# Performance work log

Measured on AMD Instinct MI355X. Metric: run time of the kernel, lower is better.

Reference implementation:

```python
import jax, jax.numpy as jnp
import numpy as np

HIDDEN = 1024
B, S = 4, 2048


def setup_inputs() -> dict:
    key = jax.random.key(0)
    ks = jax.random.split(key, 8)
    scale = 1.0 / np.sqrt(HIDDEN)
    return {
        "hidden_states": jax.random.normal(ks[0], (B, S, HIDDEN), dtype=jnp.float32),
        "attention_mask": jnp.zeros((B, S, S), dtype=jnp.float32),
        "Wq": jax.random.normal(ks[1], (HIDDEN, HIDDEN), dtype=jnp.float32) * scale,
        "bq": jnp.zeros((HIDDEN,), dtype=jnp.float32),
        "Wk": jax.random.normal(ks[2], (HIDDEN, HIDDEN), dtype=jnp.float32) * scale,
        "bk": jnp.zeros((HIDDEN,), dtype=jnp.float32),
        "Wv": jax.random.normal(ks[3], (HIDDEN, HIDDEN), dtype=jnp.float32) * scale,
        "bv": jnp.zeros((HIDDEN,), dtype=jnp.float32),
    }


def reference(hidden_states, attention_mask, Wq, bq, Wk, bk, Wv, bv):
    # Dense projections (note: no head split in the original module)
    q = jnp.einsum('bsd,de->bse', hidden_states, Wq) + bq  # [B,S,H]
    k = jnp.einsum('bsd,de->bse', hidden_states, Wk) + bk
    v = jnp.einsum('bsd,de->bse', hidden_states, Wv) + bv
    # scores scaled by sqrt(hidden_size) (not per-head dim), per the source
    inv_scale = 1.0 / jnp.sqrt(jnp.asarray(q.shape[-1], dtype=q.dtype))
    scores = jnp.einsum('bqd,bkd->bqk', q, k) * inv_scale  # [B,S,S]
    scores = scores + attention_mask
    weights = jax.nn.softmax(scores, axis=-1)
    # dropout is identity (training=False)
    out = jnp.einsum('bqk,bkd->bqd', weights, v)  # [B,S,H]
    return out
```

## Files before the change

kernel.cpp:

```cpp
#include <hip/hip_runtime.h>
#include <stdint.h>

typedef __attribute__((ext_vector_type(8))) short short8;
typedef __attribute__((ext_vector_type(8))) unsigned short u16x8;
typedef __attribute__((ext_vector_type(4))) float f32x4;

__device__ __forceinline__ uint16_t f2bf(float x) {
  uint32_t u = __float_as_uint(x);
  uint32_t r = (u + 0x7FFFu + ((u >> 16) & 1u)) >> 16;
  return (uint16_t)r;
}
__device__ __forceinline__ float bf2f(uint16_t x) {
  return __uint_as_float(((uint32_t)x) << 16);
}

__device__ __forceinline__ void gl_lds16(const uint16_t* g, void* l) {
  __builtin_amdgcn_global_load_lds(
      (const __attribute__((address_space(1))) void*)g,
      (__attribute__((address_space(3))) void*)l, 16, 0, 0);
}


__global__ __launch_bounds__(256) void cvt_f32_to_bf16(const float* __restrict__ in,
                                                       uint16_t* __restrict__ out) {
  long i = ((long)blockIdx.x * 256 + threadIdx.x) * 8;
  f32x4 v0 = *(const f32x4*)(in + i);
  f32x4 v1 = *(const f32x4*)(in + i + 4);
  u16x8 o;
  o[0] = f2bf(v0[0]); o[1] = f2bf(v0[1]); o[2] = f2bf(v0[2]); o[3] = f2bf(v0[3]);
  o[4] = f2bf(v1[0]); o[5] = f2bf(v1[1]); o[6] = f2bf(v1[2]); o[7] = f2bf(v1[3]);
  *(u16x8*)(out + i) = o;
}

__global__ __launch_bounds__(64) void cvt_w_transpose(const float* __restrict__ W0,
                                                      const float* __restrict__ W1,
                                                      const float* __restrict__ W2,
                                                      uint16_t* __restrict__ WT) {
  const int z = blockIdx.z;
  const float* W = (z == 0) ? W0 : ((z == 1) ? W1 : W2);
  uint16_t* out = WT + (long)z * 1024 * 1024;
  const int n = blockIdx.x * 64 + threadIdx.x;
  const int k0 = blockIdx.y * 128;
  for (int kk = 0; kk < 128; kk += 8) {
    u16x8 o;
#pragma unroll
    for (int j = 0; j < 8; j++) o[j] = f2bf(W[(long)(k0 + kk + j) * 1024 + n]);
    *(u16x8*)(out + (long)n * 1024 + k0 + kk) = o;
  }
}

__global__ __launch_bounds__(256) void transpose_v(const uint16_t* __restrict__ V,
                                                   uint16_t* __restrict__ Vt) {
  __shared__ uint16_t tile[64][66];
  const int b = blockIdx.z;
  const int s0 = blockIdx.x * 64, d0 = blockIdx.y * 64;
  const int t = threadIdx.x;
  const int r = t >> 3, c = (t & 7) * 8;
  const uint16_t* Vb = V + (long)b * 2048 * 1024;
#pragma unroll
  for (int j = 0; j < 2; j++) {
    u16x8 v = *(const u16x8*)(Vb + (long)(s0 + r + 32 * j) * 1024 + d0 + c);
#pragma unroll
    for (int i = 0; i < 8; i++) tile[r + 32 * j][c + i] = v[i];
  }
  __syncthreads();
  uint16_t* Vtb = Vt + (long)b * 1024 * 2048;
#pragma unroll
  for (int j = 0; j < 2; j++) {
    const int d = r + 32 * j;
    u16x8 o;
#pragma unroll
    for (int i = 0; i < 8; i++) o[i] = tile[c + i][d];
    *(u16x8*)(Vtb + (long)(d0 + d) * 2048 + s0 + c) = o;
  }
}

__global__ __launch_bounds__(256) void rowsum_inv(const uint16_t* __restrict__ E,
                                                  float* __restrict__ invl) {
  const long row = blockIdx.x;
  const uint16_t* src = E + row * 2048;
  const int t = threadIdx.x;
  u16x8 v = *(const u16x8*)(src + t * 8);
  float s = 0.f;
#pragma unroll
  for (int i = 0; i < 8; i++) s += bf2f(v[i]);
#pragma unroll
  for (int off = 32; off >= 1; off >>= 1) s += __shfl_xor(s, off);
  __shared__ float red[4];
  if ((t & 63) == 0) red[t >> 6] = s;
  __syncthreads();
  if (t == 0) {
    invl[row] = 1.0f / (red[0] + red[1] + red[2] + red[3]);
  }
}

template <int MODE>
__global__ __launch_bounds__(512, 2) void gemm256(
    const uint16_t* __restrict__ Abase, long sAz,
    const uint16_t* __restrict__ Bbase, long sBz,
    int K, int N,
    char* __restrict__ Cbase, long sCz,
    const float* __restrict__ e0, const float* __restrict__ e1,
    const float* __restrict__ e2,
    const float* __restrict__ maskb, long sMz, float scale) {
  __shared__ __align__(16) char lds[131072];
  const int t = threadIdx.x;
  const int lane = t & 63;
  const int w = t >> 6;
  const int bm = blockIdx.x, bn = blockIdx.y, bz = blockIdx.z;
  const uint16_t* A = (const uint16_t*)((const char*)Abase + (long)bz * sAz);
  const uint16_t* B = (const uint16_t*)((const char*)Bbase + (long)bz * sBz);

  const int srow = t >> 3;
  const int scol = ((((t & 7) * 16) ^ ((srow & 7) << 4)) >> 1);
  const uint16_t* gA[4];
  const uint16_t* gB[4];
#pragma unroll
  for (int s = 0; s < 4; s++) {
    gA[s] = A + (long)(bm * 256 + s * 64 + srow) * K + scol;
    gB[s] = B + (long)(bn * 256 + s * 64 + srow) * K + scol;
  }

  const int wm = w >> 2, wn = w & 3;
  const int fr = lane & 15, kg = lane >> 4;
  const int X = (fr & 7) << 4;
  const int aRow = (wm * 128 + fr) * 128 + kg * 16;
  const int bRow = (wn * 64 + fr) * 128 + kg * 16;

  f32x4 acc[8][4];
#pragma unroll
  for (int i = 0; i < 8; i++)
#pragma unroll
    for (int j = 0; j < 4; j++) acc[i][j] = (f32x4){0.f, 0.f, 0.f, 0.f};

  short8 aR[4][2], bR[2][2];
  const int NT = K >> 6;

#define ARD(off, i, ks) (*(const short8*)(lds + (off) + ((aRow + (i) * 2048 + (ks) * 64) ^ X)))
#define BRD(off, j, ks) (*(const short8*)(lds + 32768 + (off) + ((bRow + (j) * 2048 + (ks) * 64) ^ X)))
#define STG_A01(off, ko) { gl_lds16(gA[0] + (ko), lds + (off) + w * 1024); \
                           gl_lds16(gA[1] + (ko), lds + (off) + 8192 + w * 1024); }
#define STG_A23(off, ko) { gl_lds16(gA[2] + (ko), lds + (off) + 16384 + w * 1024); \
                           gl_lds16(gA[3] + (ko), lds + (off) + 24576 + w * 1024); }
#define STG_B01(off, ko) { gl_lds16(gB[0] + (ko), lds + 32768 + (off) + w * 1024); \
                           gl_lds16(gB[1] + (ko), lds + 32768 + (off) + 8192 + w * 1024); }
#define STG_B23(off, ko) { gl_lds16(gB[2] + (ko), lds + 32768 + (off) + 16384 + w * 1024); \
                           gl_lds16(gB[3] + (ko), lds + 32768 + (off) + 24576 + w * 1024); }
#define LGKM0 { asm volatile("s_waitcnt lgkmcnt(0)" ::: "memory"); __builtin_amdgcn_sched_barrier(0); }
#define MFMA16(I0, J0)                                                            \
  __builtin_amdgcn_s_setprio(1);                                                  \
  _Pragma("unroll") for (int i = 0; i < 4; i++)                                   \
  _Pragma("unroll") for (int j = 0; j < 2; j++)                                   \
  _Pragma("unroll") for (int ks = 0; ks < 2; ks++)                                \
    acc[(I0) + i][(J0) + j] = __builtin_amdgcn_mfma_f32_16x16x32_bf16(            \
        aR[i][ks], bR[j][ks], acc[(I0) + i][(J0) + j], 0, 0, 0);                  \
  __builtin_amdgcn_s_setprio(0);

  STG_A01(0, 0); STG_A23(0, 0); STG_B01(0, 0); STG_B23(0, 0);

  int curo = 0;
  for (int tt = 0; tt < NT - 1; ++tt) {
    const int nxto = curo ^ 65536;
    const int ko = (tt + 1) << 6;
    STG_A01(nxto, ko);
    asm volatile("s_waitcnt vmcnt(2)" ::: "memory");
    __builtin_amdgcn_s_barrier();
    __builtin_amdgcn_sched_barrier(0);
#pragma unroll
    for (int i = 0; i < 4; i++) { aR[i][0] = ARD(curo, i, 0); aR[i][1] = ARD(curo, i, 1); }
#pragma unroll
    for (int j = 0; j < 2; j++) { bR[j][0] = BRD(curo, j, 0); bR[j][1] = BRD(curo, j, 1); }
    LGKM0;
    MFMA16(0, 0);
    __builtin_amdgcn_s_barrier();
    STG_A23(nxto, ko);
#pragma unroll
    for (int j = 0; j < 2; j++) { bR[j][0] = BRD(curo, 2 + j, 0); bR[j][1] = BRD(curo, 2 + j, 1); }
    __builtin_amdgcn_s_barrier();
    LGKM0;
    MFMA16(0, 2);
    __builtin_amdgcn_s_barrier();
    STG_B01(nxto, ko);
#pragma unroll
    for (int i = 0; i < 4; i++) { aR[i][0] = ARD(curo, 4 + i, 0); aR[i][1] = ARD(curo, 4 + i, 1); }
    __builtin_amdgcn_s_barrier();
    LGKM0;
    MFMA16(4, 2);
    __builtin_amdgcn_s_barrier();
    STG_B23(nxto, ko);
#pragma unroll
    for (int j = 0; j < 2; j++) { bR[j][0] = BRD(curo, j, 0); bR[j][1] = BRD(curo, j, 1); }
    __builtin_amdgcn_s_barrier();
    LGKM0;
    MFMA16(4, 0);
    __builtin_amdgcn_s_barrier();
    curo = nxto;
  }
  asm volatile("s_waitcnt vmcnt(0)" ::: "memory");
  __builtin_amdgcn_s_barrier();
  __builtin_amdgcn_sched_barrier(0);
#pragma unroll
  for (int i = 0; i < 4; i++) { aR[i][0] = ARD(curo, i, 0); aR[i][1] = ARD(curo, i, 1); }
#pragma unroll
  for (int j = 0; j < 2; j++) { bR[j][0] = BRD(curo, j, 0); bR[j][1] = BRD(curo, j, 1); }
  LGKM0;
  MFMA16(0, 0);
#pragma unroll
  for (int j = 0; j < 2; j++) { bR[j][0] = BRD(curo, 2 + j, 0); bR[j][1] = BRD(curo, 2 + j, 1); }
  LGKM0;
  MFMA16(0, 2);
#pragma unroll
  for (int i = 0; i < 4; i++) { aR[i][0] = ARD(curo, 4 + i, 0); aR[i][1] = ARD(curo, 4 + i, 1); }
  LGKM0;
  MFMA16(4, 2);
#pragma unroll
  for (int j = 0; j < 2; j++) { bR[j][0] = BRD(curo, j, 0); bR[j][1] = BRD(curo, j, 1); }
  LGKM0;
  MFMA16(4, 0);

  const int row0 = bm * 256 + wm * 128 + (kg << 2);
  const int col0 = bn * 256 + wn * 64 + fr;
  if (MODE == 0) {
    const float* bias = (bz == 0) ? e0 : ((bz == 1) ? e1 : e2);
    uint16_t* C = (uint16_t*)(Cbase + (long)bz * sCz);
#pragma unroll
    for (int i = 0; i < 8; i++) {
#pragma unroll
      for (int j = 0; j < 4; j++) {
        const float bv_ = bias[col0 + j * 16];
#pragma unroll
        for (int r = 0; r < 4; r++) {
          C[(long)(row0 + i * 16 + r) * N + col0 + j * 16] = f2bf(acc[i][j][r] + bv_);
        }
      }
    }
  } else {
    uint16_t* C = (uint16_t*)(Cbase + (long)bz * sCz);
    const float* mk = (const float*)((const char*)maskb + (long)bz * sMz);
#pragma unroll
    for (int i = 0; i < 8; i++) {
#pragma unroll
      for (int j = 0; j < 4; j++) {
#pragma unroll
        for (int r = 0; r < 4; r++) {
          const long idx = (long)(row0 + i * 16 + r) * N + col0 + j * 16;
          C[idx] = f2bf(__expf(acc[i][j][r] * scale + mk[idx]));
        }
      }
    }
  }
#undef ARD
#undef BRD
#undef STG_A01
#undef STG_A23
#undef STG_B01
#undef STG_B23
#undef LGKM0
#undef MFMA16
}

__global__ __launch_bounds__(256) void gemm_pv(
    const uint16_t* __restrict__ Abase, long sAz,
    const uint16_t* __restrict__ Bbase, long sBz,
    int K, int N,
    float* __restrict__ Cbase, long sCzf,
    const float* __restrict__ rowinv) {
  __shared__ uint16_t Al[2][128 * 32];
  __shared__ uint16_t Bl[2][128 * 32];
  const int t = threadIdx.x;
  const int lane = t & 63;
  const int w = t >> 6;
  const int bm = blockIdx.x, bn = blockIdx.y, bz = blockIdx.z;

  const uint16_t* A = (const uint16_t*)((const char*)Abase + (long)bz * sAz);
  const uint16_t* Bm = (const uint16_t*)((const char*)Bbase + (long)bz * sBz);

  const int sr = t >> 2;
  const int sc = (t & 3) * 8;
  const uint16_t* ga0 = A + (long)(bm * 128 + sr) * K + sc;
  const uint16_t* ga1 = A + (long)(bm * 128 + 64 + sr) * K + sc;
  const uint16_t* gb0 = Bm + (long)(bn * 128 + sr) * K + sc;
  const uint16_t* gb1 = Bm + (long)(bn * 128 + 64 + sr) * K + sc;

  f32x4 acc[4][4];
#pragma unroll
  for (int i = 0; i < 4; i++)
#pragma unroll
    for (int j = 0; j < 4; j++) acc[i][j] = (f32x4){0.f, 0.f, 0.f, 0.f};

  const int wm = w >> 1, wn = w & 1;
  const int fr = lane & 15, kg = lane >> 4;
  const int aoff = (wm * 64 + fr) * 32 + kg * 8;
  const int boff = (wn * 64 + fr) * 32 + kg * 8;

  gl_lds16(ga0, Al[0] + w * 512);
  gl_lds16(ga1, Al[0] + 2048 + w * 512);
  gl_lds16(gb0, Bl[0] + w * 512);
  gl_lds16(gb1, Bl[0] + 2048 + w * 512);

  int cur = 0;
  for (int k0 = 0; k0 < K; k0 += 32) {
    __syncthreads();
    if (k0 + 32 < K) {
      const int nb = cur ^ 1, kn = k0 + 32;
      gl_lds16(ga0 + kn, Al[nb] + w * 512);
      gl_lds16(ga1 + kn, Al[nb] + 2048 + w * 512);
      gl_lds16(gb0 + kn, Bl[nb] + w * 512);
      gl_lds16(gb1 + kn, Bl[nb] + 2048 + w * 512);
    }
    const uint16_t* Ab = Al[cur];
    const uint16_t* Bb = Bl[cur];
    short8 a[4], b[4];
#pragma unroll
    for (int i = 0; i < 4; i++) a[i] = *(const short8*)(Ab + aoff + i * 16 * 32);
#pragma unroll
    for (int j = 0; j < 4; j++) b[j] = *(const short8*)(Bb + boff + j * 16 * 32);
#pragma unroll
    for (int i = 0; i < 4; i++)
#pragma unroll
      for (int j = 0; j < 4; j++)
        acc[i][j] = __builtin_amdgcn_mfma_f32_16x16x32_bf16(a[i], b[j], acc[i][j], 0, 0, 0);
    cur ^= 1;
  }

  const int row0 = bm * 128 + wm * 64 + (kg << 2);
  const int col0 = bn * 128 + wn * 64 + fr;
  float* C = Cbase + (long)bz * sCzf;
  const float* ri = rowinv + (long)bz * 2048;
#pragma unroll
  for (int i = 0; i < 4; i++) {
#pragma unroll
    for (int j = 0; j < 4; j++) {
#pragma unroll
      for (int r = 0; r < 4; r++) {
        const int row = row0 + i * 16 + r;
        C[(long)row * N + col0 + j * 16] = acc[i][j][r] * ri[row];
      }
    }
  }
}

extern "C" void kernel_launch(void* const* d_in, const int* in_sizes, int n_in,
                              void* d_out, int out_size, void* d_ws, size_t ws_size,
                              hipStream_t stream) {
  const float* hs = (const float*)d_in[0];
  const float* mask = (const float*)d_in[1];
  const float* Wq = (const float*)d_in[2];
  const float* bq = (const float*)d_in[3];
  const float* Wk = (const float*)d_in[4];
  const float* bk = (const float*)d_in[5];
  const float* Wv = (const float*)d_in[6];
  const float* bv = (const float*)d_in[7];
  float* out = (float*)d_out;

  char* ws = (char*)d_ws;
  uint16_t* hsb = (uint16_t*)ws;
  uint16_t* WT = (uint16_t*)(ws + (16L << 20));
  uint16_t* QKV = (uint16_t*)(ws + (22L << 20));
  uint16_t* Vt = (uint16_t*)(ws + (70L << 20));
  uint16_t* E = (uint16_t*)(ws + (86L << 20));
  float* invl = (float*)(ws + (118L << 20));

  cvt_f32_to_bf16<<<4096, 256, 0, stream>>>(hs, hsb);
  cvt_w_transpose<<<dim3(16, 8, 3), 64, 0, stream>>>(Wq, Wk, Wv, WT);
  gemm256<0><<<dim3(32, 4, 3), 512, 0, stream>>>(
      hsb, 0L, WT, 2L << 20, 1024, 1024, (char*)QKV, 16L << 20,
      bq, bk, bv, nullptr, 0L, 0.f);
  transpose_v<<<dim3(32, 16, 4), 256, 0, stream>>>(QKV + 2L * 8192 * 1024, Vt);
  gemm256<1><<<dim3(8, 8, 4), 512, 0, stream>>>(
      QKV, 4L << 20, QKV + 8192L * 1024, 4L << 20, 1024, 2048, (char*)E, 8L << 20,
      nullptr, nullptr, nullptr, mask, 16L << 20, 0.03125f);
  rowsum_inv<<<8192, 256, 0, stream>>>(E, invl);
  gemm_pv<<<dim3(16, 8, 4), 256, 0, stream>>>(
      E, 8L << 20, Vt, 4L << 20, 2048, 1024, out, 2048L * 1024, invl);
}
```

Before: 204.7 us.

## Generalize 256-wide GEMM to variable M tile and reuse for QKV and PV

The 256x256 GEMM kernel is templated on the M tile height (AI), which shrinks LDS use and the accumulator count for AI=4. The QKV projection becomes one GEMM with 128x256 tiles over N=3072, treating the concatenated transposed weights as a single matrix. The old 128x128 PV GEMM is replaced by the pipelined gemmX kernel with 128x256 tiles and the row-normalization epilogue. The aim is better wave and tile utilization and a better-pipelined PV stage, at the cost of a different occupancy and schedule balance for the smaller tiles.

```diff
diff --git a/kernel.cpp b/kernel.cpp
--- a/kernel.cpp
+++ b/kernel.cpp
@@ -94,16 +94,20 @@
   }
 }
 
-template <int MODE>
-__global__ __launch_bounds__(512, 2) void gemm256(
+template <int MODE, int AI>
+__global__ __launch_bounds__(512, 2) void gemmX(
     const uint16_t* __restrict__ Abase, long sAz,
     const uint16_t* __restrict__ Bbase, long sBz,
     int K, int N,
     char* __restrict__ Cbase, long sCz,
     const float* __restrict__ e0, const float* __restrict__ e1,
     const float* __restrict__ e2,
-    const float* __restrict__ maskb, long sMz, float scale) {
-  __shared__ __align__(16) char lds[131072];
+    const float* __restrict__ maskb, long sMz, float scale,
+    const float* __restrict__ rowinv) {
+  constexpr int BM = AI * 32;
+  constexpr int ABYTES = BM * 128;
+  constexpr int BUFB = ABYTES + 32768;
+  __shared__ __align__(16) char lds[2 * BUFB];
   const int t = threadIdx.x;
   const int lane = t & 63;
   const int w = t >> 6;
@@ -117,19 +121,19 @@
   const uint16_t* gB[4];
 #pragma unroll
   for (int s = 0; s < 4; s++) {
-    gA[s] = A + (long)(bm * 256 + s * 64 + srow) * K + scol;
+    gA[s] = A + (long)(bm * BM + (s % (AI / 2)) * 64 + srow) * K + scol;
     gB[s] = B + (long)(bn * 256 + s * 64 + srow) * K + scol;
   }
 
   const int wm = w >> 2, wn = w & 3;
   const int fr = lane & 15, kg = lane >> 4;
   const int X = (fr & 7) << 4;
-  const int aRow = (wm * 128 + fr) * 128 + kg * 16;
+  const int aRow = (wm * (AI * 16) + fr) * 128 + kg * 16;
   const int bRow = (wn * 64 + fr) * 128 + kg * 16;
 
-  f32x4 acc[8][4];
-#pragma unroll
-  for (int i = 0; i < 8; i++)
+  f32x4 acc[AI][4];
+#pragma unroll
+  for (int i = 0; i < AI; i++)
 #pragma unroll
     for (int j = 0; j < 4; j++) acc[i][j] = (f32x4){0.f, 0.f, 0.f, 0.f};
 
@@ -137,15 +141,15 @@
   const int NT = K >> 6;
 
 #define ARD(off, i, ks) (*(const short8*)(lds + (off) + ((aRow + (i) * 2048 + (ks) * 64) ^ X)))
-#define BRD(off, j, ks) (*(const short8*)(lds + 32768 + (off) + ((bRow + (j) * 2048 + (ks) * 64) ^ X)))
+#define BRD(off, j, ks) (*(const short8*)(lds + ABYTES + (off) + ((bRow + (j) * 2048 + (ks) * 64) ^ X)))
 #define STG_A01(off, ko) { gl_lds16(gA[0] + (ko), lds + (off) + w * 1024); \
                            gl_lds16(gA[1] + (ko), lds + (off) + 8192 + w * 1024); }
 #define STG_A23(off, ko) { gl_lds16(gA[2] + (ko), lds + (off) + 16384 + w * 1024); \
                            gl_lds16(gA[3] + (ko), lds + (off) + 24576 + w * 1024); }
-#define STG_B01(off, ko) { gl_lds16(gB[0] + (ko), lds + 32768 + (off) + w * 1024); \
-                           gl_lds16(gB[1] + (ko), lds + 32768 + (off) + 8192 + w * 1024); }
-#define STG_B23(off, ko) { gl_lds16(gB[2] + (ko), lds + 32768 + (off) + 16384 + w * 1024); \
-                           gl_lds16(gB[3] + (ko), lds + 32768 + (off) + 24576 + w * 1024); }
+#define STG_B01(off, ko) { gl_lds16(gB[0] + (ko), lds + ABYTES + (off) + w * 1024); \
+                           gl_lds16(gB[1] + (ko), lds + ABYTES + (off) + 8192 + w * 1024); }
+#define STG_B23(off, ko) { gl_lds16(gB[2] + (ko), lds + ABYTES + (off) + 16384 + w * 1024); \
+                           gl_lds16(gB[3] + (ko), lds + ABYTES + (off) + 24576 + w * 1024); }
 #define LGKM0 { asm volatile("s_waitcnt lgkmcnt(0)" ::: "memory"); __builtin_amdgcn_sched_barrier(0); }
 #define MFMA16(I0, J0)                                                            \
   __builtin_amdgcn_s_setprio(1);                                                  \
@@ -156,95 +160,149 @@
         aR[i][ks], bR[j][ks], acc[(I0) + i][(J0) + j], 0, 0, 0);                  \
   __builtin_amdgcn_s_setprio(0);
 
-  STG_A01(0, 0); STG_A23(0, 0); STG_B01(0, 0); STG_B23(0, 0);
+  if constexpr (AI == 8) { STG_A01(0, 0); STG_A23(0, 0); }
+  else                   { STG_A01(0, 0); }
+  STG_B01(0, 0); STG_B23(0, 0);
 
   int curo = 0;
   for (int tt = 0; tt < NT - 1; ++tt) {
-    const int nxto = curo ^ 65536;
+    const int nxto = curo ^ BUFB;
     const int ko = (tt + 1) << 6;
-    STG_A01(nxto, ko);
-    asm volatile("s_waitcnt vmcnt(2)" ::: "memory");
-    __builtin_amdgcn_s_barrier();
-    __builtin_amdgcn_sched_barrier(0);
-#pragma unroll
-    for (int i = 0; i < 4; i++) { aR[i][0] = ARD(curo, i, 0); aR[i][1] = ARD(curo, i, 1); }
-#pragma unroll
-    for (int j = 0; j < 2; j++) { bR[j][0] = BRD(curo, j, 0); bR[j][1] = BRD(curo, j, 1); }
-    LGKM0;
-    MFMA16(0, 0);
-    __builtin_amdgcn_s_barrier();
-    STG_A23(nxto, ko);
-#pragma unroll
-    for (int j = 0; j < 2; j++) { bR[j][0] = BRD(curo, 2 + j, 0); bR[j][1] = BRD(curo, 2 + j, 1); }
-    __builtin_amdgcn_s_barrier();
-    LGKM0;
-    MFMA16(0, 2);
-    __builtin_amdgcn_s_barrier();
-    STG_B01(nxto, ko);
-#pragma unroll
-    for (int i = 0; i < 4; i++) { aR[i][0] = ARD(curo, 4 + i, 0); aR[i][1] = ARD(curo, 4 + i, 1); }
-    __builtin_amdgcn_s_barrier();
-    LGKM0;
-    MFMA16(4, 2);
-    __builtin_amdgcn_s_barrier();
-    STG_B23(nxto, ko);
-#pragma unroll
-    for (int j = 0; j < 2; j++) { bR[j][0] = BRD(curo, j, 0); bR[j][1] = BRD(curo, j, 1); }
-    __builtin_amdgcn_s_barrier();
-    LGKM0;
-    MFMA16(4, 0);
-    __builtin_amdgcn_s_barrier();
+    if constexpr (AI == 8) {
+      STG_A01(nxto, ko);
+      asm volatile("s_waitcnt vmcnt(2)" ::: "memory");
+      __builtin_amdgcn_s_barrier();
+      __builtin_amdgcn_sched_barrier(0);
+#pragma unroll
+      for (int i = 0; i < 4; i++) { aR[i][0] = ARD(curo, i, 0); aR[i][1] = ARD(curo, i, 1); }
+#pragma unroll
+      for (int j = 0; j < 2; j++) { bR[j][0] = BRD(curo, j, 0); bR[j][1] = BRD(curo, j, 1); }
+      LGKM0;
+      MFMA16(0, 0);
+      __builtin_amdgcn_s_barrier();
+      STG_A23(nxto, ko);
+#pragma unroll
+      for (int j = 0; j < 2; j++) { bR[j][0] = BRD(curo, 2 + j, 0); bR[j][1] = BRD(curo, 2 + j, 1); }
+      __builtin_amdgcn_s_barrier();
+      LGKM0;
+      MFMA16(0, 2);
+      __builtin_amdgcn_s_barrier();
+      STG_B01(nxto, ko);
+#pragma unroll
+      for (int i = 0; i < 4; i++) { aR[i][0] = ARD(curo, 4 + i, 0); aR[i][1] = ARD(curo, 4 + i, 1); }
+      __builtin_amdgcn_s_barrier();
+      LGKM0;
+      MFMA16(4, 2);
+      __builtin_amdgcn_s_barrier();
+      STG_B23(nxto, ko);
+#pragma unroll
+      for (int j = 0; j < 2; j++) { bR[j][0] = BRD(curo, j, 0); bR[j][1] = BRD(curo, j, 1); }
+      __builtin_amdgcn_s_barrier();
+      LGKM0;
+      MFMA16(4, 0);
+      __builtin_amdgcn_s_barrier();
+    } else {
+      STG_A01(nxto, ko);
+      STG_B01(nxto, ko);
+      asm volatile("s_waitcnt vmcnt(4)" ::: "memory");
+      __builtin_amdgcn_s_barrier();
+      __builtin_amdgcn_sched_barrier(0);
+#pragma unroll
+      for (int i = 0; i < 4; i++) { aR[i][0] = ARD(curo, i, 0); aR[i][1] = ARD(curo, i, 1); }
+#pragma unroll
+      for (int j = 0; j < 2; j++) { bR[j][0] = BRD(curo, j, 0); bR[j][1] = BRD(curo, j, 1); }
+      LGKM0;
+      MFMA16(0, 0);
+      __builtin_amdgcn_s_barrier();
+      STG_B23(nxto, ko);
+#pragma unroll
+      for (int j = 0; j < 2; j++) { bR[j][0] = BRD(curo, 2 + j, 0); bR[j][1] = BRD(curo, 2 + j, 1); }
+      __builtin_amdgcn_s_barrier();
+      LGKM0;
+      MFMA16(0, 2);
+      __builtin_amdgcn_s_barrier();
+    }
     curo = nxto;
   }
   asm volatile("s_waitcnt vmcnt(0)" ::: "memory");
   __builtin_amdgcn_s_barrier();
   __builtin_amdgcn_sched_barrier(0);
-#pragma unroll
-  for (int i = 0; i < 4; i++) { aR[i][0] = ARD(curo, i, 0); aR[i][1] = ARD(curo, i, 1); }
-#pragma unroll
-  for (int j = 0; j < 2; j++) { bR[j][0] = BRD(curo, j, 0); bR[j][1] = BRD(curo, j, 1); }
-  LGKM0;
-  MFMA16(0, 0);
-#pragma unroll
-  for (int j = 0; j < 2; j++) { bR[j][0] = BRD(curo, 2 + j, 0); bR[j][1] = BRD(curo, 2 + j, 1); }
-  LGKM0;
-  MFMA16(0, 2);
-#pragma unroll
-  for (int i = 0; i < 4; i++) { aR[i][0] = ARD(curo, 4 + i, 0); aR[i][1] = ARD(curo, 4 + i, 1); }
-  LGKM0;
-  MFMA16(4, 2);
-#pragma unroll
-  for (int j = 0; j < 2; j++) { bR[j][0] = BRD(curo, j, 0); bR[j][1] = BRD(curo, j, 1); }
-  LGKM0;
-  MFMA16(4, 0);
-
-  const int row0 = bm * 256 + wm * 128 + (kg << 2);
-  const int col0 = bn * 256 + wn * 64 + fr;
+  if constexpr (AI == 8) {
+#pragma unroll
+    for (int i = 0; i < 4; i++) { aR[i][0] = ARD(curo, i, 0); aR[i][1] = ARD(curo, i, 1); }
+#pragma unroll
+    for (int j = 0; j < 2; j++) { bR[j][0] = BRD(curo, j, 0); bR[j][1] = BRD(curo, j, 1); }
+    LGKM0;
+    MFMA16(0, 0);
+#pragma unroll
+    for (int j = 0; j < 2; j++) { bR[j][0] = BRD(curo, 2 + j, 0); bR[j][1] = BRD(curo, 2 + j, 1); }
+    LGKM0;
+    MFMA16(0, 2);
+#pragma unroll
+    for (int i = 0; i < 4; i++) { aR[i][0] = ARD(curo, 4 + i, 0); aR[i][1] = ARD(curo, 4 + i, 1); }
+    LGKM0;
+    MFMA16(4, 2);
+#pragma unroll
+    for (int j = 0; j < 2; j++) { bR[j][0] = BRD(curo, j, 0); bR[j][1] = BRD(curo, j, 1); }
+    LGKM0;
+    MFMA16(4, 0);
+  } else {
+#pragma unroll
+    for (int i = 0; i < 4; i++) { aR[i][0] = ARD(curo, i, 0); aR[i][1] = ARD(curo, i, 1); }
+#pragma unroll
+    for (int j = 0; j < 2; j++) { bR[j][0] = BRD(curo, j, 0); bR[j][1] = BRD(curo, j, 1); }
+    LGKM0;
+    MFMA16(0, 0);
+#pragma unroll
+    for (int j = 0; j < 2; j++) { bR[j][0] = BRD(curo, 2 + j, 0); bR[j][1] = BRD(curo, 2 + j, 1); }
+    LGKM0;
+    MFMA16(0, 2);
+  }
+
+  const int row0 = bm * BM + wm * (AI * 16) + (kg << 2);
   if (MODE == 0) {
-    const float* bias = (bz == 0) ? e0 : ((bz == 1) ? e1 : e2);
+    const int zz = bn >> 2;
+    const float* bias = (zz == 0) ? e0 : ((zz == 1) ? e1 : e2);
+    uint16_t* C = (uint16_t*)(Cbase + (long)zz * sCz);
+    const int cb = (bn & 3) * 256 + wn * 64 + fr;
+#pragma unroll
+    for (int i = 0; i < AI; i++) {
+#pragma unroll
+      for (int j = 0; j < 4; j++) {
+        const float bv_ = bias[cb + j * 16];
+#pragma unroll
+        for (int r = 0; r < 4; r++) {
+          C[(long)(row0 + i * 16 + r) * 1024 + cb + j * 16] = f2bf(acc[i][j][r] + bv_);
+        }
+      }
+    }
+  } else if (MODE == 1) {
+    const int col0 = bn * 256 + wn * 64 + fr;
     uint16_t* C = (uint16_t*)(Cbase + (long)bz * sCz);
-#pragma unroll
-    for (int i = 0; i < 8; i++) {
+    const float* mk = (const float*)((const char*)maskb + (long)bz * sMz);
+#pragma unroll
+    for (int i = 0; i < AI; i++) {
 #pragma unroll
       for (int j = 0; j < 4; j++) {
-        const float bv_ = bias[col0 + j * 16];
 #pragma unroll
         for (int r = 0; r < 4; r++) {
-          C[(long)(row0 + i * 16 + r) * N + col0 + j * 16] = f2bf(acc[i][j][r] + bv_);
+          const long idx = (long)(row0 + i * 16 + r) * N + col0 + j * 16;
+          C[idx] = f2bf(__expf(acc[i][j][r] * scale + mk[idx]));
         }
       }
     }
   } else {
-    uint16_t* C = (uint16_t*)(Cbase + (long)bz * sCz);
-    const float* mk = (const float*)((const char*)maskb + (long)bz * sMz);
-#pragma unroll
-    for (int i = 0; i < 8; i++) {
+    const int col0 = bn * 256 + wn * 64 + fr;
+    float* C = (float*)(Cbase + (long)bz * sCz);
+    const float* ri = rowinv + (long)bz * 2048;
+#pragma unroll
+    for (int i = 0; i < AI; i++) {
 #pragma unroll
       for (int j = 0; j < 4; j++) {
 #pragma unroll
         for (int r = 0; r < 4; r++) {
-          const long idx = (long)(row0 + i * 16 + r) * N + col0 + j * 16;
-          C[idx] = f2bf(__expf(acc[i][j][r] * scale + mk[idx]));
+          const int row = row0 + i * 16 + r;
+          C[(long)row * N + col0 + j * 16] = acc[i][j][r] * ri[row];
         }
       }
     }
@@ -257,87 +315,6 @@
 #undef STG_B23
 #undef LGKM0
 #undef MFMA16
-}
-
-__global__ __launch_bounds__(256) void gemm_pv(
-    const uint16_t* __restrict__ Abase, long sAz,
-    const uint16_t* __restrict__ Bbase, long sBz,
-    int K, int N,
-    float* __restrict__ Cbase, long sCzf,
-    const float* __restrict__ rowinv) {
-  __shared__ uint16_t Al[2][128 * 32];
-  __shared__ uint16_t Bl[2][128 * 32];
-  const int t = threadIdx.x;
-  const int lane = t & 63;
-  const int w = t >> 6;
-  const int bm = blockIdx.x, bn = blockIdx.y, bz = blockIdx.z;
-
-  const uint16_t* A = (const uint16_t*)((const char*)Abase + (long)bz * sAz);
-  const uint16_t* Bm = (const uint16_t*)((const char*)Bbase + (long)bz * sBz);
-
-  const int sr = t >> 2;
-  const int sc = (t & 3) * 8;
-  const uint16_t* ga0 = A + (long)(bm * 128 + sr) * K + sc;
-  const uint16_t* ga1 = A + (long)(bm * 128 + 64 + sr) * K + sc;
-  const uint16_t* gb0 = Bm + (long)(bn * 128 + sr) * K + sc;
-  const uint16_t* gb1 = Bm + (long)(bn * 128 + 64 + sr) * K + sc;
-
-  f32x4 acc[4][4];
-#pragma unroll
-  for (int i = 0; i < 4; i++)
-#pragma unroll
-    for (int j = 0; j < 4; j++) acc[i][j] = (f32x4){0.f, 0.f, 0.f, 0.f};
-
-  const int wm = w >> 1, wn = w & 1;
-  const int fr = lane & 15, kg = lane >> 4;
-  const int aoff = (wm * 64 + fr) * 32 + kg * 8;
-  const int boff = (wn * 64 + fr) * 32 + kg * 8;
-
-  gl_lds16(ga0, Al[0] + w * 512);
-  gl_lds16(ga1, Al[0] + 2048 + w * 512);
-  gl_lds16(gb0, Bl[0] + w * 512);
-  gl_lds16(gb1, Bl[0] + 2048 + w * 512);
-
-  int cur = 0;
-  for (int k0 = 0; k0 < K; k0 += 32) {
-    __syncthreads();
-    if (k0 + 32 < K) {
-      const int nb = cur ^ 1, kn = k0 + 32;
-      gl_lds16(ga0 + kn, Al[nb] + w * 512);
-      gl_lds16(ga1 + kn, Al[nb] + 2048 + w * 512);
-      gl_lds16(gb0 + kn, Bl[nb] + w * 512);
-      gl_lds16(gb1 + kn, Bl[nb] + 2048 + w * 512);
-    }
-    const uint16_t* Ab = Al[cur];
-    const uint16_t* Bb = Bl[cur];
-    short8 a[4], b[4];
-#pragma unroll
-    for (int i = 0; i < 4; i++) a[i] = *(const short8*)(Ab + aoff + i * 16 * 32);
-#pragma unroll
-    for (int j = 0; j < 4; j++) b[j] = *(const short8*)(Bb + boff + j * 16 * 32);
-#pragma unroll
-    for (int i = 0; i < 4; i++)
-#pragma unroll
-      for (int j = 0; j < 4; j++)
-        acc[i][j] = __builtin_amdgcn_mfma_f32_16x16x32_bf16(a[i], b[j], acc[i][j], 0, 0, 0);
-    cur ^= 1;
-  }
-
-  const int row0 = bm * 128 + wm * 64 + (kg << 2);
-  const int col0 = bn * 128 + wn * 64 + fr;
-  float* C = Cbase + (long)bz * sCzf;
-  const float* ri = rowinv + (long)bz * 2048;
-#pragma unroll
-  for (int i = 0; i < 4; i++) {
-#pragma unroll
-    for (int j = 0; j < 4; j++) {
-#pragma unroll
-      for (int r = 0; r < 4; r++) {
-        const int row = row0 + i * 16 + r;
-        C[(long)row * N + col0 + j * 16] = acc[i][j][r] * ri[row];
-      }
-    }
-  }
 }
 
 extern "C" void kernel_launch(void* const* d_in, const int* in_sizes, int n_in,
@@ -363,14 +340,15 @@
 
   cvt_f32_to_bf16<<<4096, 256, 0, stream>>>(hs, hsb);
   cvt_w_transpose<<<dim3(16, 8, 3), 64, 0, stream>>>(Wq, Wk, Wv, WT);
-  gemm256<0><<<dim3(32, 4, 3), 512, 0, stream>>>(
-      hsb, 0L, WT, 2L << 20, 1024, 1024, (char*)QKV, 16L << 20,
-      bq, bk, bv, nullptr, 0L, 0.f);
+  gemmX<0, 4><<<dim3(64, 12, 1), 512, 0, stream>>>(
+      hsb, 0L, WT, 0L, 1024, 3072, (char*)QKV, 16L << 20,
+      bq, bk, bv, nullptr, 0L, 0.f, nullptr);
   transpose_v<<<dim3(32, 16, 4), 256, 0, stream>>>(QKV + 2L * 8192 * 1024, Vt);
-  gemm256<1><<<dim3(8, 8, 4), 512, 0, stream>>>(
+  gemmX<1, 8><<<dim3(8, 8, 4), 512, 0, stream>>>(
       QKV, 4L << 20, QKV + 8192L * 1024, 4L << 20, 1024, 2048, (char*)E, 8L << 20,
-      nullptr, nullptr, nullptr, mask, 16L << 20, 0.03125f);
+      nullptr, nullptr, nullptr, mask, 16L << 20, 0.03125f, nullptr);
   rowsum_inv<<<8192, 256, 0, stream>>>(E, invl);
-  gemm_pv<<<dim3(16, 8, 4), 256, 0, stream>>>(
-      E, 8L << 20, Vt, 4L << 20, 2048, 1024, out, 2048L * 1024, invl);
-}
+  gemmX<2, 4><<<dim3(16, 4, 4), 512, 0, stream>>>(
+      E, 8L << 20, Vt, 4L << 20, 2048, 1024, (char*)out, 8L << 20,
+      nullptr, nullptr, nullptr, nullptr, 0L, 0.f, invl);
+}
```

Result: faster. 191.5 us (-6.4%).

## Fuse softmax row-sum into score GEMM epilogue and restructure GEMM kernels

Applied to the files above, without the earlier changes.

The score GEMM epilogue now stages its accumulators through LDS so each thread can read contiguous rows. It applies the mask and exp with vectorized loads and stores, and accumulates per-row sums with shuffles and atomicAdd. This removes the separate rowsum_inv pass over E. The QKV projection now runs on the smaller 128x128 gemm_pv-style kernel instead of the 256x256 one, and the score kernel keeps all four B fragments in registers to drop two LDS read phases per iteration. Costs added are a memset, atomics, per-element reciprocal divides in the PV epilogue, and more register pressure.

```diff
diff --git a/kernel.cpp b/kernel.cpp
--- a/kernel.cpp
+++ b/kernel.cpp
@@ -75,196 +75,15 @@
   }
 }
 
-__global__ __launch_bounds__(256) void rowsum_inv(const uint16_t* __restrict__ E,
-                                                  float* __restrict__ invl) {
-  const long row = blockIdx.x;
-  const uint16_t* src = E + row * 2048;
-  const int t = threadIdx.x;
-  u16x8 v = *(const u16x8*)(src + t * 8);
-  float s = 0.f;
-#pragma unroll
-  for (int i = 0; i < 8; i++) s += bf2f(v[i]);
-#pragma unroll
-  for (int off = 32; off >= 1; off >>= 1) s += __shfl_xor(s, off);
-  __shared__ float red[4];
-  if ((t & 63) == 0) red[t >> 6] = s;
-  __syncthreads();
-  if (t == 0) {
-    invl[row] = 1.0f / (red[0] + red[1] + red[2] + red[3]);
-  }
-}
-
 template <int MODE>
-__global__ __launch_bounds__(512, 2) void gemm256(
+__global__ __launch_bounds__(256) void gemm_bt(
     const uint16_t* __restrict__ Abase, long sAz,
     const uint16_t* __restrict__ Bbase, long sBz,
     int K, int N,
     char* __restrict__ Cbase, long sCz,
     const float* __restrict__ e0, const float* __restrict__ e1,
     const float* __restrict__ e2,
-    const float* __restrict__ maskb, long sMz, float scale) {
-  __shared__ __align__(16) char lds[131072];
-  const int t = threadIdx.x;
-  const int lane = t & 63;
-  const int w = t >> 6;
-  const int bm = blockIdx.x, bn = blockIdx.y, bz = blockIdx.z;
-  const uint16_t* A = (const uint16_t*)((const char*)Abase + (long)bz * sAz);
-  const uint16_t* B = (const uint16_t*)((const char*)Bbase + (long)bz * sBz);
-
-  const int srow = t >> 3;
-  const int scol = ((((t & 7) * 16) ^ ((srow & 7) << 4)) >> 1);
-  const uint16_t* gA[4];
-  const uint16_t* gB[4];
-#pragma unroll
-  for (int s = 0; s < 4; s++) {
-    gA[s] = A + (long)(bm * 256 + s * 64 + srow) * K + scol;
-    gB[s] = B + (long)(bn * 256 + s * 64 + srow) * K + scol;
-  }
-
-  const int wm = w >> 2, wn = w & 3;
-  const int fr = lane & 15, kg = lane >> 4;
-  const int X = (fr & 7) << 4;
-  const int aRow = (wm * 128 + fr) * 128 + kg * 16;
-  const int bRow = (wn * 64 + fr) * 128 + kg * 16;
-
-  f32x4 acc[8][4];
-#pragma unroll
-  for (int i = 0; i < 8; i++)
-#pragma unroll
-    for (int j = 0; j < 4; j++) acc[i][j] = (f32x4){0.f, 0.f, 0.f, 0.f};
-
-  short8 aR[4][2], bR[2][2];
-  const int NT = K >> 6;
-
-#define ARD(off, i, ks) (*(const short8*)(lds + (off) + ((aRow + (i) * 2048 + (ks) * 64) ^ X)))
-#define BRD(off, j, ks) (*(const short8*)(lds + 32768 + (off) + ((bRow + (j) * 2048 + (ks) * 64) ^ X)))
-#define STG_A01(off, ko) { gl_lds16(gA[0] + (ko), lds + (off) + w * 1024); \
-                           gl_lds16(gA[1] + (ko), lds + (off) + 8192 + w * 1024); }
-#define STG_A23(off, ko) { gl_lds16(gA[2] + (ko), lds + (off) + 16384 + w * 1024); \
-                           gl_lds16(gA[3] + (ko), lds + (off) + 24576 + w * 1024); }
-#define STG_B01(off, ko) { gl_lds16(gB[0] + (ko), lds + 32768 + (off) + w * 1024); \
-                           gl_lds16(gB[1] + (ko), lds + 32768 + (off) + 8192 + w * 1024); }
-#define STG_B23(off, ko) { gl_lds16(gB[2] + (ko), lds + 32768 + (off) + 16384 + w * 1024); \
-                           gl_lds16(gB[3] + (ko), lds + 32768 + (off) + 24576 + w * 1024); }
-#define LGKM0 { asm volatile("s_waitcnt lgkmcnt(0)" ::: "memory"); __builtin_amdgcn_sched_barrier(0); }
-#define MFMA16(I0, J0)                                                            \
-  __builtin_amdgcn_s_setprio(1);                                                  \
-  _Pragma("unroll") for (int i = 0; i < 4; i++)                                   \
-  _Pragma("unroll") for (int j = 0; j < 2; j++)                                   \
-  _Pragma("unroll") for (int ks = 0; ks < 2; ks++)                                \
-    acc[(I0) + i][(J0) + j] = __builtin_amdgcn_mfma_f32_16x16x32_bf16(            \
-        aR[i][ks], bR[j][ks], acc[(I0) + i][(J0) + j], 0, 0, 0);                  \
-  __builtin_amdgcn_s_setprio(0);
-
-  STG_A01(0, 0); STG_A23(0, 0); STG_B01(0, 0); STG_B23(0, 0);
-
-  int curo = 0;
-  for (int tt = 0; tt < NT - 1; ++tt) {
-    const int nxto = curo ^ 65536;
-    const int ko = (tt + 1) << 6;
-    STG_A01(nxto, ko);
-    asm volatile("s_waitcnt vmcnt(2)" ::: "memory");
-    __builtin_amdgcn_s_barrier();
-    __builtin_amdgcn_sched_barrier(0);
-#pragma unroll
-    for (int i = 0; i < 4; i++) { aR[i][0] = ARD(curo, i, 0); aR[i][1] = ARD(curo, i, 1); }
-#pragma unroll
-    for (int j = 0; j < 2; j++) { bR[j][0] = BRD(curo, j, 0); bR[j][1] = BRD(curo, j, 1); }
-    LGKM0;
-    MFMA16(0, 0);
-    __builtin_amdgcn_s_barrier();
-    STG_A23(nxto, ko);
-#pragma unroll
-    for (int j = 0; j < 2; j++) { bR[j][0] = BRD(curo, 2 + j, 0); bR[j][1] = BRD(curo, 2 + j, 1); }
-    __builtin_amdgcn_s_barrier();
-    LGKM0;
-    MFMA16(0, 2);
-    __builtin_amdgcn_s_barrier();
-    STG_B01(nxto, ko);
-#pragma unroll
-    for (int i = 0; i < 4; i++) { aR[i][0] = ARD(curo, 4 + i, 0); aR[i][1] = ARD(curo, 4 + i, 1); }
-    __builtin_amdgcn_s_barrier();
-    LGKM0;
-    MFMA16(4, 2);
-    __builtin_amdgcn_s_barrier();
-    STG_B23(nxto, ko);
-#pragma unroll
-    for (int j = 0; j < 2; j++) { bR[j][0] = BRD(curo, j, 0); bR[j][1] = BRD(curo, j, 1); }
-    __builtin_amdgcn_s_barrier();
-    LGKM0;
-    MFMA16(4, 0);
-    __builtin_amdgcn_s_barrier();
-    curo = nxto;
-  }
-  asm volatile("s_waitcnt vmcnt(0)" ::: "memory");
-  __builtin_amdgcn_s_barrier();
-  __builtin_amdgcn_sched_barrier(0);
-#pragma unroll
-  for (int i = 0; i < 4; i++) { aR[i][0] = ARD(curo, i, 0); aR[i][1] = ARD(curo, i, 1); }
-#pragma unroll
-  for (int j = 0; j < 2; j++) { bR[j][0] = BRD(curo, j, 0); bR[j][1] = BRD(curo, j, 1); }
-  LGKM0;
-  MFMA16(0, 0);
-#pragma unroll
-  for (int j = 0; j < 2; j++) { bR[j][0] = BRD(curo, 2 + j, 0); bR[j][1] = BRD(curo, 2 + j, 1); }
-  LGKM0;
-  MFMA16(0, 2);
-#pragma unroll
-  for (int i = 0; i < 4; i++) { aR[i][0] = ARD(curo, 4 + i, 0); aR[i][1] = ARD(curo, 4 + i, 1); }
-  LGKM0;
-  MFMA16(4, 2);
-#pragma unroll
-  for (int j = 0; j < 2; j++) { bR[j][0] = BRD(curo, j, 0); bR[j][1] = BRD(curo, j, 1); }
-  LGKM0;
-  MFMA16(4, 0);
-
-  const int row0 = bm * 256 + wm * 128 + (kg << 2);
-  const int col0 = bn * 256 + wn * 64 + fr;
-  if (MODE == 0) {
-    const float* bias = (bz == 0) ? e0 : ((bz == 1) ? e1 : e2);
-    uint16_t* C = (uint16_t*)(Cbase + (long)bz * sCz);
-#pragma unroll
-    for (int i = 0; i < 8; i++) {
-#pragma unroll
-      for (int j = 0; j < 4; j++) {
-        const float bv_ = bias[col0 + j * 16];
-#pragma unroll
-        for (int r = 0; r < 4; r++) {
-          C[(long)(row0 + i * 16 + r) * N + col0 + j * 16] = f2bf(acc[i][j][r] + bv_);
-        }
-      }
-    }
-  } else {
-    uint16_t* C = (uint16_t*)(Cbase + (long)bz * sCz);
-    const float* mk = (const float*)((const char*)maskb + (long)bz * sMz);
-#pragma unroll
-    for (int i = 0; i < 8; i++) {
-#pragma unroll
-      for (int j = 0; j < 4; j++) {
-#pragma unroll
-        for (int r = 0; r < 4; r++) {
-          const long idx = (long)(row0 + i * 16 + r) * N + col0 + j * 16;
-          C[idx] = f2bf(__expf(acc[i][j][r] * scale + mk[idx]));
-        }
-      }
-    }
-  }
-#undef ARD
-#undef BRD
-#undef STG_A01
-#undef STG_A23
-#undef STG_B01
-#undef STG_B23
-#undef LGKM0
-#undef MFMA16
-}
-
-__global__ __launch_bounds__(256) void gemm_pv(
-    const uint16_t* __restrict__ Abase, long sAz,
-    const uint16_t* __restrict__ Bbase, long sBz,
-    int K, int N,
-    float* __restrict__ Cbase, long sCzf,
-    const float* __restrict__ rowinv) {
+    const float* __restrict__ lsum) {
   __shared__ uint16_t Al[2][128 * 32];
   __shared__ uint16_t Bl[2][128 * 32];
   const int t = threadIdx.x;
@@ -325,19 +144,215 @@
 
   const int row0 = bm * 128 + wm * 64 + (kg << 2);
   const int col0 = bn * 128 + wn * 64 + fr;
-  float* C = Cbase + (long)bz * sCzf;
-  const float* ri = rowinv + (long)bz * 2048;
-#pragma unroll
-  for (int i = 0; i < 4; i++) {
-#pragma unroll
-    for (int j = 0; j < 4; j++) {
-#pragma unroll
-      for (int r = 0; r < 4; r++) {
-        const int row = row0 + i * 16 + r;
-        C[(long)row * N + col0 + j * 16] = acc[i][j][r] * ri[row];
+
+  if (MODE == 0) {
+    const float* bias = (bz == 0) ? e0 : ((bz == 1) ? e1 : e2);
+    uint16_t* C = (uint16_t*)(Cbase + (long)bz * sCz);
+#pragma unroll
+    for (int i = 0; i < 4; i++) {
+#pragma unroll
+      for (int j = 0; j < 4; j++) {
+        const float bv_ = bias[col0 + j * 16];
+#pragma unroll
+        for (int r = 0; r < 4; r++) {
+          C[(long)(row0 + i * 16 + r) * N + col0 + j * 16] = f2bf(acc[i][j][r] + bv_);
+        }
       }
     }
-  }
+  } else {
+    float* C = (float*)(Cbase + (long)bz * sCz);
+    const float* ls = lsum + (long)bz * 2048;
+#pragma unroll
+    for (int i = 0; i < 4; i++) {
+      const float ri0 = 1.0f / ls[row0 + i * 16];
+      const float ri1 = 1.0f / ls[row0 + i * 16 + 1];
+      const float ri2 = 1.0f / ls[row0 + i * 16 + 2];
+      const float ri3 = 1.0f / ls[row0 + i * 16 + 3];
+#pragma unroll
+      for (int j = 0; j < 4; j++) {
+        float* dst = C + (long)(row0 + i * 16) * N + col0 + j * 16;
+        dst[0] = acc[i][j][0] * ri0;
+        dst[(long)N] = acc[i][j][1] * ri1;
+        dst[(long)2 * N] = acc[i][j][2] * ri2;
+        dst[(long)3 * N] = acc[i][j][3] * ri3;
+      }
+    }
+  }
+}
+
+__global__ __launch_bounds__(512, 2) void gemm_sc(
+    const uint16_t* __restrict__ Abase, long sAz,
+    const uint16_t* __restrict__ Bbase, long sBz,
+    int K, int N,
+    char* __restrict__ Cbase, long sCz,
+    const float* __restrict__ maskb, long sMz, float scale,
+    float* __restrict__ lsum) {
+  constexpr int ABYTES = 32768;
+  constexpr int BUFB = 65536;
+  __shared__ __align__(16) char lds[2 * BUFB];
+  const int t = threadIdx.x;
+  const int lane = t & 63;
+  const int w = t >> 6;
+  const int bm = blockIdx.x, bn = blockIdx.y, bz = blockIdx.z;
+  const uint16_t* A = (const uint16_t*)((const char*)Abase + (long)bz * sAz);
+  const uint16_t* B = (const uint16_t*)((const char*)Bbase + (long)bz * sBz);
+
+  const int srow = t >> 3;
+  const int scol = ((((t & 7) * 16) ^ ((srow & 7) << 4)) >> 1);
+  const uint16_t* gA[4];
+  const uint16_t* gB[4];
+#pragma unroll
+  for (int s = 0; s < 4; s++) {
+    gA[s] = A + (long)(bm * 256 + s * 64 + srow) * K + scol;
+    gB[s] = B + (long)(bn * 256 + s * 64 + srow) * K + scol;
+  }
+
+  const int wm = w >> 2, wn = w & 3;
+  const int fr = lane & 15, kg = lane >> 4;
+  const int X = (fr & 7) << 4;
+  const int aRow = (wm * 128 + fr) * 128 + kg * 16;
+  const int bRow = (wn * 64 + fr) * 128 + kg * 16;
+
+  f32x4 acc[8][4];
+#pragma unroll
+  for (int i = 0; i < 8; i++)
+#pragma unroll
+    for (int j = 0; j < 4; j++) acc[i][j] = (f32x4){0.f, 0.f, 0.f, 0.f};
+
+  short8 aR[4][2], bR[4][2];
+  const int NT = K >> 6;
+
+#define ARD(off, i, ks) (*(const short8*)(lds + (off) + ((aRow + (i) * 2048 + (ks) * 64) ^ X)))
+#define BRD(off, j, ks) (*(const short8*)(lds + ABYTES + (off) + ((bRow + (j) * 2048 + (ks) * 64) ^ X)))
+#define STG_A01(off, ko) { gl_lds16(gA[0] + (ko), lds + (off) + w * 1024); \
+                           gl_lds16(gA[1] + (ko), lds + (off) + 8192 + w * 1024); }
+#define STG_A23(off, ko) { gl_lds16(gA[2] + (ko), lds + (off) + 16384 + w * 1024); \
+                           gl_lds16(gA[3] + (ko), lds + (off) + 24576 + w * 1024); }
+#define STG_B01(off, ko) { gl_lds16(gB[0] + (ko), lds + ABYTES + (off) + w * 1024); \
+                           gl_lds16(gB[1] + (ko), lds + ABYTES + (off) + 8192 + w * 1024); }
+#define STG_B23(off, ko) { gl_lds16(gB[2] + (ko), lds + ABYTES + (off) + 16384 + w * 1024); \
+                           gl_lds16(gB[3] + (ko), lds + ABYTES + (off) + 24576 + w * 1024); }
+#define LGKM0 { asm volatile("s_waitcnt lgkmcnt(0)" ::: "memory"); __builtin_amdgcn_sched_barrier(0); }
+#define MFMA16(I0, J0)                                                            \
+  __builtin_amdgcn_s_setprio(1);                                                  \
+  _Pragma("unroll") for (int i = 0; i < 4; i++)                                   \
+  _Pragma("unroll") for (int j = 0; j < 2; j++)                                   \
+  _Pragma("unroll") for (int ks = 0; ks < 2; ks++)                                \
+    acc[(I0) + i][(J0) + j] = __builtin_amdgcn_mfma_f32_16x16x32_bf16(            \
+        aR[i][ks], bR[(J0) + j][ks], acc[(I0) + i][(J0) + j], 0, 0, 0);           \
+  __builtin_amdgcn_s_setprio(0);
+
+  STG_A01(0, 0); STG_A23(0, 0); STG_B01(0, 0); STG_B23(0, 0);
+
+  int curo = 0;
+  for (int tt = 0; tt < NT - 1; ++tt) {
+    const int nxto = curo ^ BUFB;
+    const int ko = (tt + 1) << 6;
+    STG_A01(nxto, ko);
+    asm volatile("s_waitcnt vmcnt(2)" ::: "memory");
+    __builtin_amdgcn_s_barrier();
+    __builtin_amdgcn_sched_barrier(0);
+#pragma unroll
+    for (int i = 0; i < 4; i++) { aR[i][0] = ARD(curo, i, 0); aR[i][1] = ARD(curo, i, 1); }
+#pragma unroll
+    for (int j = 0; j < 4; j++) { bR[j][0] = BRD(curo, j, 0); bR[j][1] = BRD(curo, j, 1); }
+    LGKM0;
+    MFMA16(0, 0);
+    __builtin_amdgcn_s_barrier();
+    STG_A23(nxto, ko);
+    __builtin_amdgcn_s_barrier();
+    MFMA16(0, 2);
+    __builtin_amdgcn_s_barrier();
+    STG_B01(nxto, ko);
+#pragma unroll
+    for (int i = 0; i < 4; i++) { aR[i][0] = ARD(curo, 4 + i, 0); aR[i][1] = ARD(curo, 4 + i, 1); }
+    __builtin_amdgcn_s_barrier();
+    LGKM0;
+    MFMA16(4, 2);
+    __builtin_amdgcn_s_barrier();
+    STG_B23(nxto, ko);
+    __builtin_amdgcn_s_barrier();
+    MFMA16(4, 0);
+    __builtin_amdgcn_s_barrier();
+    curo = nxto;
+  }
+  asm volatile("s_waitcnt vmcnt(0)" ::: "memory");
+  __builtin_amdgcn_s_barrier();
+  __builtin_amdgcn_sched_barrier(0);
+#pragma unroll
+  for (int i = 0; i < 4; i++) { aR[i][0] = ARD(curo, i, 0); aR[i][1] = ARD(curo, i, 1); }
+#pragma unroll
+  for (int j = 0; j < 4; j++) { bR[j][0] = BRD(curo, j, 0); bR[j][1] = BRD(curo, j, 1); }
+  LGKM0;
+  MFMA16(0, 0);
+  MFMA16(0, 2);
+#pragma unroll
+  for (int i = 0; i < 4; i++) { aR[i][0] = ARD(curo, 4 + i, 0); aR[i][1] = ARD(curo, 4 + i, 1); }
+  LGKM0;
+  MFMA16(4, 2);
+  MFMA16(4, 0);
+
+  __syncthreads();
+  constexpr int RS = 260;
+  float* eL = (float*)lds;
+  const int wboff = wm * (16 * RS) + (kg * 4) * RS + wn * 64 + fr;
+  const int lr = t >> 4, slab = lr >> 4, row16 = lr & 15, cj = t & 15;
+  const float* rb = eL + slab * (16 * RS) + row16 * RS + cj * 16;
+  const int grow_base = bm * 256 + slab * 128 + row16;
+  const int colg = bn * 256 + cj * 16;
+  uint16_t* Cw = (uint16_t*)(Cbase + (long)bz * sCz);
+  const float* mk = (const float*)((const char*)maskb + (long)bz * sMz);
+
+#pragma unroll
+  for (int i = 0; i < 8; i++) {
+#pragma unroll
+    for (int j = 0; j < 4; j++)
+#pragma unroll
+      for (int r = 0; r < 4; r++)
+        eL[wboff + r * RS + j * 16] = acc[i][j][r];
+    __syncthreads();
+    f32x4 v0 = *(const f32x4*)(rb);
+    f32x4 v1 = *(const f32x4*)(rb + 4);
+    f32x4 v2 = *(const f32x4*)(rb + 8);
+    f32x4 v3 = *(const f32x4*)(rb + 12);
+    const int grow = grow_base + i * 16;
+    const float* mrow = mk + (long)grow * N + colg;
+    f32x4 m0 = *(const f32x4*)(mrow);
+    f32x4 m1 = *(const f32x4*)(mrow + 4);
+    f32x4 m2 = *(const f32x4*)(mrow + 8);
+    f32x4 m3 = *(const f32x4*)(mrow + 12);
+    float e[16];
+#pragma unroll
+    for (int q = 0; q < 4; q++) {
+      e[q] = __expf(v0[q] * scale + m0[q]);
+      e[4 + q] = __expf(v1[q] * scale + m1[q]);
+      e[8 + q] = __expf(v2[q] * scale + m2[q]);
+      e[12 + q] = __expf(v3[q] * scale + m3[q]);
+    }
+    float ps = 0.f;
+#pragma unroll
+    for (int q = 0; q < 16; q++) ps += e[q];
+    ps += __shfl_xor(ps, 1);
+    ps += __shfl_xor(ps, 2);
+    ps += __shfl_xor(ps, 4);
+    ps += __shfl_xor(ps, 8);
+    if ((lane & 15) == 0) atomicAdd(lsum + (long)bz * 2048 + grow, ps);
+    u16x8 o0, o1;
+#pragma unroll
+    for (int q = 0; q < 8; q++) { o0[q] = f2bf(e[q]); o1[q] = f2bf(e[8 + q]); }
+    uint16_t* dst = Cw + (long)grow * N + colg;
+    *(u16x8*)dst = o0;
+    *(u16x8*)(dst + 8) = o1;
+    __syncthreads();
+  }
+#undef ARD
+#undef BRD
+#undef STG_A01
+#undef STG_A23
+#undef STG_B01
+#undef STG_B23
+#undef LGKM0
+#undef MFMA16
 }
 
 extern "C" void kernel_launch(void* const* d_in, const int* in_sizes, int n_in,
@@ -359,18 +374,19 @@
   uint16_t* QKV = (uint16_t*)(ws + (22L << 20));
   uint16_t* Vt = (uint16_t*)(ws + (70L << 20));
   uint16_t* E = (uint16_t*)(ws + (86L << 20));
-  float* invl = (float*)(ws + (118L << 20));
+  float* lsum = (float*)(ws + (118L << 20));
 
   cvt_f32_to_bf16<<<4096, 256, 0, stream>>>(hs, hsb);
   cvt_w_transpose<<<dim3(16, 8, 3), 64, 0, stream>>>(Wq, Wk, Wv, WT);
-  gemm256<0><<<dim3(32, 4, 3), 512, 0, stream>>>(
+  hipMemsetAsync((void*)lsum, 0, 4L * 2048 * sizeof(float), stream);
+  gemm_bt<0><<<dim3(64, 8, 3), 256, 0, stream>>>(
       hsb, 0L, WT, 2L << 20, 1024, 1024, (char*)QKV, 16L << 20,
-      bq, bk, bv, nullptr, 0L, 0.f);
+      bq, bk, bv, nullptr);
   transpose_v<<<dim3(32, 16, 4), 256, 0, stream>>>(QKV + 2L * 8192 * 1024, Vt);
-  gemm256<1><<<dim3(8, 8, 4), 512, 0, stream>>>(
+  gemm_sc<<<dim3(8, 8, 4), 512, 0, stream>>>(
       QKV, 4L << 20, QKV + 8192L * 1024, 4L << 20, 1024, 2048, (char*)E, 8L << 20,
-      nullptr, nullptr, nullptr, mask, 16L << 20, 0.03125f);
-  rowsum_inv<<<8192, 256, 0, stream>>>(E, invl);
-  gemm_pv<<<dim3(16, 8, 4), 256, 0, stream>>>(
-      E, 8L << 20, Vt, 4L << 20, 2048, 1024, out, 2048L * 1024, invl);
-}
+      mask, 16L << 20, 0.03125f, lsum);
+  gemm_bt<2><<<dim3(16, 8, 4), 256, 0, stream>>>(
+      E, 8L << 20, Vt, 4L << 20, 2048, 1024, (char*)out, 8L << 20,
+      nullptr, nullptr, nullptr, lsum);
+}
```

Result: faster. 196.5 us (-4.0%).
